# Kernel optimization log

Measured on AMD Instinct MI355X. Metric: run time of the kernel, lower is better.

Reference implementation:

```python
import jax, jax.numpy as jnp
import numpy as np

N_NODES = 50000
N_EDGES = 800000
D_IN = 128
D_OUT = 128


def setup_inputs() -> dict:
    key = jax.random.key(0)
    k_x, k_r, k_c, k_v, k_w = jax.random.split(key, 5)
    x = jax.random.normal(k_x, (N_NODES, D_IN), dtype=jnp.float32)
    edge_row = jax.random.randint(k_r, (N_EDGES,), 0, N_NODES)  # destination nodes
    edge_col = jax.random.randint(k_c, (N_EDGES,), 0, N_NODES)  # source nodes
    edge_val = jax.random.uniform(k_v, (N_EDGES,), dtype=jnp.float32)
    W = jax.random.normal(k_w, (D_OUT, D_IN), dtype=jnp.float32) * (1.0 / np.sqrt(D_IN))
    bias = jnp.zeros((D_OUT,), dtype=jnp.float32)
    return {"x": x, "edge_row": edge_row, "edge_col": edge_col,
            "edge_val": edge_val, "W": W, "bias": bias}


def reference(x, edge_row, edge_col, edge_val, W, bias):
    # support = linear(x)   (nn.Linear with bias=False: x @ W.T)
    support = jnp.einsum('ni,oi->no', x, W)  # [N, D_OUT]
    # out = sparse.mm(adj, support): gather source rows, scale by edge value,
    # scatter-add into destination rows.
    msgs = edge_val[:, None] * support[edge_col]  # [E, D_OUT]
    out = jax.ops.segment_sum(msgs, edge_row, num_segments=N_NODES)
    return out + bias
```

## Files before the change

kernel.cpp:

```cpp
#include <hip/hip_runtime.h>
#include <hip/hip_bf16.h>


constexpr int D     = 128;
constexpr int NPB   = 64;
constexpr int CAP   = 2048;
constexpr int C1    = 2048;
constexpr int BT    = 1024;
constexpr int NBMAX = 1024;

__device__ inline unsigned int bf1(float f) {
    unsigned int u = __float_as_uint(f);
    return (u + 0x7fffu + ((u >> 16) & 1u)) >> 16;
}
__device__ inline unsigned int cvt2(float a, float b) {
    __hip_bfloat162 h = __float22bfloat162_rn(float2{a, b});
    return *reinterpret_cast<unsigned int*>(&h);
}
__device__ inline float bflo(unsigned int u) { return __uint_as_float(u << 16); }
__device__ inline float bfhi(unsigned int u) { return __uint_as_float(u & 0xffff0000u); }

__global__ __launch_bounds__(256) void fused_gemm_bin_kernel(
        const float* __restrict__ x, const float* __restrict__ W,
        const int* __restrict__ erow, const int* __restrict__ ecol,
        const float* __restrict__ eval,
        int* __restrict__ gcursor, int2* __restrict__ coarse,
        unsigned short* __restrict__ supb,
        int n_edges, int nb, int n_nodes, int bin_blocks) {
    if ((int)blockIdx.x < bin_blocks) {
        __shared__ int bkcnt[NBMAX];
        __shared__ int bkoff[NBMAX];
        __shared__ int wsum[4];
        __shared__ int gbase[NBMAX];
        __shared__ unsigned short slotbk[C1];
        __shared__ int2 stage[C1];
        const int t = threadIdx.x;
        const int base = blockIdx.x * C1;
        const int m = min(C1, n_edges - base);

        for (int i = t; i < NBMAX; i += 256) bkcnt[i] = 0;
        __syncthreads();

        constexpr int EPT = C1 / 256;
        int  bk[EPT], rank[EPT];
        int2 pk[EPT];
#pragma unroll
        for (int j = 0; j < EPT; ++j) {
            int i = t + j * 256;
            bk[j] = -1;
            if (i < m) {
                int e = base + i;
                int dst = erow[e];
                int b = dst / NPB;
                bk[j] = b;
                rank[j] = atomicAdd(&bkcnt[b], 1);
                pk[j] = make_int2(ecol[e] | ((dst & (NPB - 1)) << 20),
                                  __float_as_int(eval[e]));
            }
        }
        __syncthreads();

        {
            const int w = t >> 6, l = t & 63;
            const int b0 = 4 * t;
            int c0 = bkcnt[b0], c1 = bkcnt[b0 + 1];
            int c2 = bkcnt[b0 + 2], c3 = bkcnt[b0 + 3];
            int s = c0 + c1 + c2 + c3;
            int inc = s;
#pragma unroll
            for (int o = 1; o < 64; o <<= 1) {
                int u = __shfl_up(inc, o, 64);
                if (l >= o) inc += u;
            }
            if (l == 63) wsum[w] = inc;
            __syncthreads();
            if (t < 4) {
                int v = wsum[t];
                int winc = v;
#pragma unroll
                for (int o = 1; o < 4; o <<= 1) {
                    int u = __shfl_up(winc, o, 4);
                    if (t >= o) winc += u;
                }
                wsum[t] = winc - v;
            }
            __syncthreads();
            int p = inc - s + wsum[w];
            bkoff[b0]     = p;
            bkoff[b0 + 1] = p + c0;
            bkoff[b0 + 2] = p + c0 + c1;
            bkoff[b0 + 3] = p + c0 + c1 + c2;
        }
        __syncthreads();

#pragma unroll
        for (int j = 0; j < EPT; ++j) {
            if (bk[j] >= 0) {
                int s2 = bkoff[bk[j]] + rank[j];
                stage[s2] = pk[j];
                slotbk[s2] = (unsigned short)bk[j];
            }
        }
        for (int i = t; i < nb; i += 256) {
            int c = bkcnt[i];
            gbase[i] = (c > 0) ? (i * CAP + atomicAdd(&gcursor[i], c)) : 0;
        }
        __syncthreads();

        for (int i = t; i < m; i += 256) {
            int b = slotbk[i];
            int p = gbase[b] + (i - bkoff[b]);
            if (p < (b + 1) * CAP) coarse[p] = stage[i];
        }
    } else {
        using frag  = __attribute__((ext_vector_type(8))) short;
        using f32x4 = __attribute__((ext_vector_type(4))) float;
        union FU { uint4 u; frag f; };
        const int wv = threadIdx.x >> 6;
        const int lane = threadIdx.x & 63;
        const int mm = lane & 15, quad = lane >> 4;
        const int row0 = (blockIdx.x - bin_blocks) * 128 + wv * 32;
        const int r0 = min(row0 + mm, n_nodes - 1);
        const int r1 = min(row0 + 16 + mm, n_nodes - 1);

        frag a0[4], a1[4];
#pragma unroll
        for (int kf = 0; kf < 4; ++kf) {
            const float4* xp0 = (const float4*)(x + (size_t)r0 * D + kf * 32 + quad * 8);
            float4 p = xp0[0], q = xp0[1];
            FU t;
            t.u.x = cvt2(p.x, p.y); t.u.y = cvt2(p.z, p.w);
            t.u.z = cvt2(q.x, q.y); t.u.w = cvt2(q.z, q.w);
            a0[kf] = t.f;
            const float4* xp1 = (const float4*)(x + (size_t)r1 * D + kf * 32 + quad * 8);
            p = xp1[0]; q = xp1[1];
            t.u.x = cvt2(p.x, p.y); t.u.y = cvt2(p.z, p.w);
            t.u.z = cvt2(q.x, q.y); t.u.w = cvt2(q.z, q.w);
            a1[kf] = t.f;
        }

        f32x4 acc0[8], acc1[8];
#pragma unroll
        for (int ct = 0; ct < 8; ++ct) {
            acc0[ct] = (f32x4){0.f, 0.f, 0.f, 0.f};
            acc1[ct] = (f32x4){0.f, 0.f, 0.f, 0.f};
        }

#pragma unroll
        for (int ct = 0; ct < 8; ++ct) {
            const float* wrow = W + (size_t)(ct * 16 + mm) * D;
#pragma unroll
            for (int kf = 0; kf < 4; ++kf) {
                const float4* wp = (const float4*)(wrow + kf * 32 + quad * 8);
                float4 p = wp[0], q = wp[1];
                FU tb;
                tb.u.x = cvt2(p.x, p.y); tb.u.y = cvt2(p.z, p.w);
                tb.u.z = cvt2(q.x, q.y); tb.u.w = cvt2(q.z, q.w);
                frag b = tb.f;
                acc0[ct] = __builtin_amdgcn_mfma_f32_16x16x32_bf16(a0[kf], b, acc0[ct], 0, 0, 0);
                acc1[ct] = __builtin_amdgcn_mfma_f32_16x16x32_bf16(a1[kf], b, acc1[ct], 0, 0, 0);
            }
        }

#pragma unroll
        for (int ct = 0; ct < 8; ++ct) {
#pragma unroll
            for (int r = 0; r < 4; ++r) {
                int rr0 = row0 + quad * 4 + r;
                if (rr0 < n_nodes)
                    supb[(size_t)rr0 * D + ct * 16 + mm] = (unsigned short)bf1(acc0[ct][r]);
                int rr1 = row0 + 16 + quad * 4 + r;
                if (rr1 < n_nodes)
                    supb[(size_t)rr1 * D + ct * 16 + mm] = (unsigned short)bf1(acc1[ct][r]);
            }
        }
    }
}

__global__ __launch_bounds__(BT) void sortgather_kernel(const int* __restrict__ gcursor,
                                                        const int2* __restrict__ coarse,
                                                        const unsigned short* __restrict__ supb,
                                                        const float* __restrict__ bias,
                                                        float* __restrict__ out,
                                                        int n_nodes) {
    __shared__ int ncnt[NPB];
    __shared__ int noff[NPB];
    __shared__ int ncur[NPB];
    __shared__ int2 sorted[CAP];
    const int t = threadIdx.x;
    const int b = blockIdx.x;
    const int node0 = b * NPB;
    const int m = min(gcursor[b], CAP);
    const int2* src = coarse + (size_t)b * CAP;

    if (t < NPB) ncnt[t] = 0;
    __syncthreads();

    for (int i = t; i < m; i += BT)
        atomicAdd(&ncnt[(src[i].x >> 20) & (NPB - 1)], 1);
    __syncthreads();

    if (t < NPB) {
        int v = ncnt[t];
        int inc = v;
        for (int o = 1; o < NPB; o <<= 1) {
            int u = __shfl_up(inc, o, 64);
            if (t >= o) inc += u;
        }
        noff[t] = inc - v;
        ncur[t] = inc - v;
    }
    __syncthreads();

    for (int i = t; i < m; i += BT) {
        int2 e = src[i];
        int dl = (e.x >> 20) & (NPB - 1);
        int p = atomicAdd(&ncur[dl], 1);
        sorted[p] = make_int2(e.x & 0xFFFFF, e.y);
    }
    __syncthreads();

    const int qw = t >> 4;
    const int l16 = t & 15;
    const int node = node0 + qw;
    if (node >= n_nodes) return;
    const int beg = noff[qw];
    const int end = beg + ncnt[qw];

    const float4* b4 = (const float4*)(bias + l16 * 8);
    float4 acc0 = b4[0], acc1 = b4[1];

    int e = beg;
    for (; e + 1 < end; e += 2) {
        int2 d0 = sorted[e], d1 = sorted[e + 1];
        uint4 u0 = *(const uint4*)(supb + (size_t)d0.x * D + l16 * 8);
        uint4 u1 = *(const uint4*)(supb + (size_t)d1.x * D + l16 * 8);
        float v0 = __int_as_float(d0.y), v1 = __int_as_float(d1.y);
        acc0.x += v0 * bflo(u0.x) + v1 * bflo(u1.x);
        acc0.y += v0 * bfhi(u0.x) + v1 * bfhi(u1.x);
        acc0.z += v0 * bflo(u0.y) + v1 * bflo(u1.y);
        acc0.w += v0 * bfhi(u0.y) + v1 * bfhi(u1.y);
        acc1.x += v0 * bflo(u0.z) + v1 * bflo(u1.z);
        acc1.y += v0 * bfhi(u0.z) + v1 * bfhi(u1.z);
        acc1.z += v0 * bflo(u0.w) + v1 * bflo(u1.w);
        acc1.w += v0 * bfhi(u0.w) + v1 * bfhi(u1.w);
    }
    if (e < end) {
        int2 d0 = sorted[e];
        uint4 u0 = *(const uint4*)(supb + (size_t)d0.x * D + l16 * 8);
        float v0 = __int_as_float(d0.y);
        acc0.x += v0 * bflo(u0.x); acc0.y += v0 * bfhi(u0.x);
        acc0.z += v0 * bflo(u0.y); acc0.w += v0 * bfhi(u0.y);
        acc1.x += v0 * bflo(u0.z); acc1.y += v0 * bfhi(u0.z);
        acc1.z += v0 * bflo(u0.w); acc1.w += v0 * bfhi(u0.w);
    }
    float4* o4 = (float4*)(out + (size_t)node * D + l16 * 8);
    o4[0] = acc0;
    o4[1] = acc1;
}

__global__ __launch_bounds__(256) void init_out_kernel(float4* __restrict__ out4,
                                                       const float4* __restrict__ bias4,
                                                       int total4) {
    int i = blockIdx.x * 256 + threadIdx.x;
    if (i < total4) out4[i] = bias4[i & 31];
}

__global__ __launch_bounds__(256) void scatter_fb_kernel(const int* __restrict__ erow,
                                                         const int* __restrict__ ecol,
                                                         const float* __restrict__ eval,
                                                         const unsigned short* __restrict__ supb,
                                                         float* __restrict__ out,
                                                         int n_edges) {
    int e = blockIdx.x * 8 + (threadIdx.x >> 5);
    if (e >= n_edges) return;
    int lane = threadIdx.x & 31;
    int src = ecol[e], dst = erow[e];
    float v = eval[e];
    const unsigned short* sp = supb + (size_t)src * D + lane * 4;
    float* op = out + (size_t)dst * D + lane * 4;
#pragma unroll
    for (int j = 0; j < 4; ++j)
        atomicAdd(op + j, v * __uint_as_float(((unsigned)sp[j]) << 16));
}

static inline size_t align_up(size_t v, size_t a) { return (v + a - 1) & ~(a - 1); }

extern "C" void kernel_launch(void* const* d_in, const int* in_sizes, int n_in,
                              void* d_out, int out_size, void* d_ws, size_t ws_size,
                              hipStream_t stream) {
    const float* x    = (const float*)d_in[0];
    const int*   erow = (const int*)d_in[1];
    const int*   ecol = (const int*)d_in[2];
    const float* eval = (const float*)d_in[3];
    const float* W    = (const float*)d_in[4];
    const float* bias = (const float*)d_in[5];
    float* out = (float*)d_out;

    const int n_nodes = in_sizes[0] / D;
    const int n_edges = in_sizes[1];
    const int nb = (n_nodes + NPB - 1) / NPB;

    char* base = (char*)d_ws;
    size_t off = 0;
    unsigned short* supb = (unsigned short*)(base + off); off = align_up(off + (size_t)n_nodes * D * 2, 256);
    int*  gcursor = (int*)(base + off);  off = align_up(off + (size_t)nb * 4, 256);
    int2* coarse  = (int2*)(base + off); off = align_up(off + (size_t)nb * CAP * 8, 256);

    const bool fast = (n_nodes < (1 << 20)) && (nb <= NBMAX) && (off <= ws_size);
    const int gemm_blocks = (n_nodes + 127) / 128;
    const int bin_blocks = fast ? (n_edges + C1 - 1) / C1 : 0;

    if (fast)
        hipMemsetAsync(gcursor, 0, (size_t)nb * 4, stream);

    fused_gemm_bin_kernel<<<bin_blocks + gemm_blocks, 256, 0, stream>>>(
        x, W, erow, ecol, eval, gcursor, coarse, supb,
        n_edges, nb, n_nodes, bin_blocks);

    if (fast) {
        sortgather_kernel<<<nb, BT, 0, stream>>>(
            gcursor, coarse, supb, bias, out, n_nodes);
    } else {
        int total4 = n_nodes * (D / 4);
        init_out_kernel<<<(total4 + 255) / 256, 256, 0, stream>>>(
            (float4*)out, (const float4*)bias, total4);
        scatter_fb_kernel<<<(n_edges + 7) / 8, 256, 0, stream>>>(
            erow, ecol, eval, supb, out, n_edges);
    }
}
```

Before: 144.8 us.

## Replace per-node sort-and-gather with fixed-point LDS atomic accumulation

The second-stage kernel no longer counting-sorts each bin's edges by destination node. Instead every wave streams edges and accumulates scaled bf16 products into a 64x128 integer accumulator in LDS using fixed-point integer atomics, then converts to float and adds bias. This removes the histogram, scan and scatter passes and the per-node load imbalance. In exchange it adds two LDS atomics per element, uses 4-byte gathers instead of 16-byte gathers, and introduces fixed-point quantization and possible overflow for large sums.

```diff
diff --git a/kernel.cpp b/kernel.cpp
--- a/kernel.cpp
+++ b/kernel.cpp
@@ -19,6 +19,9 @@
 }
 __device__ inline float bflo(unsigned int u) { return __uint_as_float(u << 16); }
 __device__ inline float bfhi(unsigned int u) { return __uint_as_float(u & 0xffff0000u); }
+
+constexpr float FXS  = 2097152.0f;
+constexpr float FXSI = 1.0f / 2097152.0f;
 
 __global__ __launch_bounds__(256) void fused_gemm_bin_kernel(
         const float* __restrict__ x, const float* __restrict__ W,
@@ -177,86 +180,70 @@
     }
 }
 
-__global__ __launch_bounds__(BT) void sortgather_kernel(const int* __restrict__ gcursor,
-                                                        const int2* __restrict__ coarse,
-                                                        const unsigned short* __restrict__ supb,
-                                                        const float* __restrict__ bias,
-                                                        float* __restrict__ out,
-                                                        int n_nodes) {
-    __shared__ int ncnt[NPB];
-    __shared__ int noff[NPB];
-    __shared__ int ncur[NPB];
-    __shared__ int2 sorted[CAP];
+__global__ __launch_bounds__(BT) void accgather_kernel(const int* __restrict__ gcursor,
+                                                       const int2* __restrict__ coarse,
+                                                       const unsigned short* __restrict__ supb,
+                                                       const float* __restrict__ bias,
+                                                       float* __restrict__ out,
+                                                       int n_nodes) {
+    __shared__ int  acc[NPB * D];
+    __shared__ int2 elist[CAP];
     const int t = threadIdx.x;
     const int b = blockIdx.x;
     const int node0 = b * NPB;
     const int m = min(gcursor[b], CAP);
     const int2* src = coarse + (size_t)b * CAP;
 
-    if (t < NPB) ncnt[t] = 0;
+    for (int i = t; i < NPB * D / 4; i += BT)
+        ((int4*)acc)[i] = int4{0, 0, 0, 0};
+    for (int i = t; i < m; i += BT) elist[i] = src[i];
     __syncthreads();
 
-    for (int i = t; i < m; i += BT)
-        atomicAdd(&ncnt[(src[i].x >> 20) & (NPB - 1)], 1);
+    const int wv = t >> 6;
+    const int c  = t & 63;
+
+    int e = wv;
+    for (; e + 48 < m; e += 64) {
+        int2 d0 = elist[e], d1 = elist[e + 16], d2 = elist[e + 32], d3 = elist[e + 48];
+        unsigned int u0 = ((const unsigned int*)(supb + ((size_t)(d0.x & 0xFFFFF) << 7)))[c];
+        unsigned int u1 = ((const unsigned int*)(supb + ((size_t)(d1.x & 0xFFFFF) << 7)))[c];
+        unsigned int u2 = ((const unsigned int*)(supb + ((size_t)(d2.x & 0xFFFFF) << 7)))[c];
+        unsigned int u3 = ((const unsigned int*)(supb + ((size_t)(d3.x & 0xFFFFF) << 7)))[c];
+        float v0 = __int_as_float(d0.y) * FXS, v1 = __int_as_float(d1.y) * FXS;
+        float v2 = __int_as_float(d2.y) * FXS, v3 = __int_as_float(d3.y) * FXS;
+        int* a0 = acc + ((d0.x >> 20) & 63) * D + 2 * c;
+        int* a1 = acc + ((d1.x >> 20) & 63) * D + 2 * c;
+        int* a2 = acc + ((d2.x >> 20) & 63) * D + 2 * c;
+        int* a3 = acc + ((d3.x >> 20) & 63) * D + 2 * c;
+        atomicAdd(a0,     __float2int_rn(bflo(u0) * v0));
+        atomicAdd(a0 + 1, __float2int_rn(bfhi(u0) * v0));
+        atomicAdd(a1,     __float2int_rn(bflo(u1) * v1));
+        atomicAdd(a1 + 1, __float2int_rn(bfhi(u1) * v1));
+        atomicAdd(a2,     __float2int_rn(bflo(u2) * v2));
+        atomicAdd(a2 + 1, __float2int_rn(bfhi(u2) * v2));
+        atomicAdd(a3,     __float2int_rn(bflo(u3) * v3));
+        atomicAdd(a3 + 1, __float2int_rn(bfhi(u3) * v3));
+    }
+    for (; e < m; e += 16) {
+        int2 d0 = elist[e];
+        unsigned int u0 = ((const unsigned int*)(supb + ((size_t)(d0.x & 0xFFFFF) << 7)))[c];
+        float v0 = __int_as_float(d0.y) * FXS;
+        int* a0 = acc + ((d0.x >> 20) & 63) * D + 2 * c;
+        atomicAdd(a0,     __float2int_rn(bflo(u0) * v0));
+        atomicAdd(a0 + 1, __float2int_rn(bfhi(u0) * v0));
+    }
     __syncthreads();
 
-    if (t < NPB) {
-        int v = ncnt[t];
-        int inc = v;
-        for (int o = 1; o < NPB; o <<= 1) {
-            int u = __shfl_up(inc, o, 64);
-            if (t >= o) inc += u;
-        }
-        noff[t] = inc - v;
-        ncur[t] = inc - v;
-    }
-    __syncthreads();
-
-    for (int i = t; i < m; i += BT) {
-        int2 e = src[i];
-        int dl = (e.x >> 20) & (NPB - 1);
-        int p = atomicAdd(&ncur[dl], 1);
-        sorted[p] = make_int2(e.x & 0xFFFFF, e.y);
-    }
-    __syncthreads();
-
-    const int qw = t >> 4;
-    const int l16 = t & 15;
-    const int node = node0 + qw;
-    if (node >= n_nodes) return;
-    const int beg = noff[qw];
-    const int end = beg + ncnt[qw];
-
-    const float4* b4 = (const float4*)(bias + l16 * 8);
-    float4 acc0 = b4[0], acc1 = b4[1];
-
-    int e = beg;
-    for (; e + 1 < end; e += 2) {
-        int2 d0 = sorted[e], d1 = sorted[e + 1];
-        uint4 u0 = *(const uint4*)(supb + (size_t)d0.x * D + l16 * 8);
-        uint4 u1 = *(const uint4*)(supb + (size_t)d1.x * D + l16 * 8);
-        float v0 = __int_as_float(d0.y), v1 = __int_as_float(d1.y);
-        acc0.x += v0 * bflo(u0.x) + v1 * bflo(u1.x);
-        acc0.y += v0 * bfhi(u0.x) + v1 * bfhi(u1.x);
-        acc0.z += v0 * bflo(u0.y) + v1 * bflo(u1.y);
-        acc0.w += v0 * bfhi(u0.y) + v1 * bfhi(u1.y);
-        acc1.x += v0 * bflo(u0.z) + v1 * bflo(u1.z);
-        acc1.y += v0 * bfhi(u0.z) + v1 * bfhi(u1.z);
-        acc1.z += v0 * bflo(u0.w) + v1 * bflo(u1.w);
-        acc1.w += v0 * bfhi(u0.w) + v1 * bfhi(u1.w);
-    }
-    if (e < end) {
-        int2 d0 = sorted[e];
-        uint4 u0 = *(const uint4*)(supb + (size_t)d0.x * D + l16 * 8);
-        float v0 = __int_as_float(d0.y);
-        acc0.x += v0 * bflo(u0.x); acc0.y += v0 * bfhi(u0.x);
-        acc0.z += v0 * bflo(u0.y); acc0.w += v0 * bfhi(u0.y);
-        acc1.x += v0 * bflo(u0.z); acc1.y += v0 * bfhi(u0.z);
-        acc1.z += v0 * bflo(u0.w); acc1.w += v0 * bfhi(u0.w);
-    }
-    float4* o4 = (float4*)(out + (size_t)node * D + l16 * 8);
-    o4[0] = acc0;
-    o4[1] = acc1;
+    const int nvalid = min(NPB, n_nodes - node0);
+    for (int i = t; i < nvalid * (D / 4); i += BT) {
+        int node = i >> 5;
+        int q = i & 31;
+        int4 a = ((const int4*)acc)[node * 32 + q];
+        float4 bb = ((const float4*)bias)[q];
+        float4 r{(float)a.x * FXSI + bb.x, (float)a.y * FXSI + bb.y,
+                 (float)a.z * FXSI + bb.z, (float)a.w * FXSI + bb.w};
+        ((float4*)(out + (size_t)(node0 + node) * D))[q] = r;
+    }
 }
 
 __global__ __launch_bounds__(256) void init_out_kernel(float4* __restrict__ out4,
@@ -319,7 +306,7 @@
         n_edges, nb, n_nodes, bin_blocks);
 
     if (fast) {
-        sortgather_kernel<<<nb, BT, 0, stream>>>(
+        accgather_kernel<<<nb, BT, 0, stream>>>(
             gcursor, coarse, supb, bias, out, n_nodes);
     } else {
         int total4 = n_nodes * (D / 4);
```

Measured after the change: 151.1 us. 1.04x slower.

## Stage bf16 W in swizzled LDS per GEMM block and halve rows per block

Applied to the files above, without the earlier changes.

Each GEMM block now converts the full W matrix to bf16 once into shared memory, stored with an XOR swizzle, and every wave reads its B fragments from LDS. Before, every wave reloaded and reconverted W from global memory for each tile. Rows per block drop from 128 to 64 (16 per wave instead of 32), which doubles the GEMM block count and lowers per-thread register use. The bin and GEMM shared-memory layouts are merged into a union so the fused kernel's LDS footprint stays bounded. The cost is an extra barrier and more blocks, each of which converts W again.

```diff
diff --git a/kernel.cpp b/kernel.cpp
--- a/kernel.cpp
+++ b/kernel.cpp
@@ -19,6 +19,19 @@
 }
 __device__ inline float bflo(unsigned int u) { return __uint_as_float(u << 16); }
 __device__ inline float bfhi(unsigned int u) { return __uint_as_float(u & 0xffff0000u); }
+
+struct BinSmem {
+    int bkcnt[NBMAX];
+    int bkoff[NBMAX];
+    int wsum[4];
+    int gbase[NBMAX];
+    unsigned short slotbk[C1];
+    int2 stage[C1];
+};
+struct GemmSmem {
+    uint4 wb[2048];
+};
+union SmemU { BinSmem b; GemmSmem g; };
 
 __global__ __launch_bounds__(256) void fused_gemm_bin_kernel(
         const float* __restrict__ x, const float* __restrict__ W,
@@ -27,18 +40,13 @@
         int* __restrict__ gcursor, int2* __restrict__ coarse,
         unsigned short* __restrict__ supb,
         int n_edges, int nb, int n_nodes, int bin_blocks) {
+    __shared__ SmemU sm;
+    const int t = threadIdx.x;
     if ((int)blockIdx.x < bin_blocks) {
-        __shared__ int bkcnt[NBMAX];
-        __shared__ int bkoff[NBMAX];
-        __shared__ int wsum[4];
-        __shared__ int gbase[NBMAX];
-        __shared__ unsigned short slotbk[C1];
-        __shared__ int2 stage[C1];
-        const int t = threadIdx.x;
         const int base = blockIdx.x * C1;
         const int m = min(C1, n_edges - base);
 
-        for (int i = t; i < NBMAX; i += 256) bkcnt[i] = 0;
+        for (int i = t; i < NBMAX; i += 256) sm.b.bkcnt[i] = 0;
         __syncthreads();
 
         constexpr int EPT = C1 / 256;
@@ -53,7 +61,7 @@
                 int dst = erow[e];
                 int b = dst / NPB;
                 bk[j] = b;
-                rank[j] = atomicAdd(&bkcnt[b], 1);
+                rank[j] = atomicAdd(&sm.b.bkcnt[b], 1);
                 pk[j] = make_int2(ecol[e] | ((dst & (NPB - 1)) << 20),
                                   __float_as_int(eval[e]));
             }
@@ -63,8 +71,8 @@
         {
             const int w = t >> 6, l = t & 63;
             const int b0 = 4 * t;
-            int c0 = bkcnt[b0], c1 = bkcnt[b0 + 1];
-            int c2 = bkcnt[b0 + 2], c3 = bkcnt[b0 + 3];
+            int c0 = sm.b.bkcnt[b0], c1 = sm.b.bkcnt[b0 + 1];
+            int c2 = sm.b.bkcnt[b0 + 2], c3 = sm.b.bkcnt[b0 + 3];
             int s = c0 + c1 + c2 + c3;
             int inc = s;
 #pragma unroll
@@ -72,106 +80,103 @@
                 int u = __shfl_up(inc, o, 64);
                 if (l >= o) inc += u;
             }
-            if (l == 63) wsum[w] = inc;
+            if (l == 63) sm.b.wsum[w] = inc;
             __syncthreads();
             if (t < 4) {
-                int v = wsum[t];
+                int v = sm.b.wsum[t];
                 int winc = v;
 #pragma unroll
                 for (int o = 1; o < 4; o <<= 1) {
                     int u = __shfl_up(winc, o, 4);
                     if (t >= o) winc += u;
                 }
-                wsum[t] = winc - v;
+                sm.b.wsum[t] = winc - v;
             }
             __syncthreads();
-            int p = inc - s + wsum[w];
-            bkoff[b0]     = p;
-            bkoff[b0 + 1] = p + c0;
-            bkoff[b0 + 2] = p + c0 + c1;
-            bkoff[b0 + 3] = p + c0 + c1 + c2;
+            int p = inc - s + sm.b.wsum[w];
+            sm.b.bkoff[b0]     = p;
+            sm.b.bkoff[b0 + 1] = p + c0;
+            sm.b.bkoff[b0 + 2] = p + c0 + c1;
+            sm.b.bkoff[b0 + 3] = p + c0 + c1 + c2;
         }
         __syncthreads();
 
 #pragma unroll
         for (int j = 0; j < EPT; ++j) {
             if (bk[j] >= 0) {
-                int s2 = bkoff[bk[j]] + rank[j];
-                stage[s2] = pk[j];
-                slotbk[s2] = (unsigned short)bk[j];
+                int s2 = sm.b.bkoff[bk[j]] + rank[j];
+                sm.b.stage[s2] = pk[j];
+                sm.b.slotbk[s2] = (unsigned short)bk[j];
             }
         }
         for (int i = t; i < nb; i += 256) {
-            int c = bkcnt[i];
-            gbase[i] = (c > 0) ? (i * CAP + atomicAdd(&gcursor[i], c)) : 0;
+            int c = sm.b.bkcnt[i];
+            sm.b.gbase[i] = (c > 0) ? (i * CAP + atomicAdd(&gcursor[i], c)) : 0;
         }
         __syncthreads();
 
         for (int i = t; i < m; i += 256) {
-            int b = slotbk[i];
-            int p = gbase[b] + (i - bkoff[b]);
-            if (p < (b + 1) * CAP) coarse[p] = stage[i];
+            int b = sm.b.slotbk[i];
+            int p = sm.b.gbase[b] + (i - sm.b.bkoff[b]);
+            if (p < (b + 1) * CAP) coarse[p] = sm.b.stage[i];
         }
     } else {
         using frag  = __attribute__((ext_vector_type(8))) short;
         using f32x4 = __attribute__((ext_vector_type(4))) float;
         union FU { uint4 u; frag f; };
-        const int wv = threadIdx.x >> 6;
-        const int lane = threadIdx.x & 63;
+        const int gb = blockIdx.x - bin_blocks;
+        const int wv = t >> 6;
+        const int lane = t & 63;
         const int mm = lane & 15, quad = lane >> 4;
-        const int row0 = (blockIdx.x - bin_blocks) * 128 + wv * 32;
+        const int row0 = gb * 64 + wv * 16;
         const int r0 = min(row0 + mm, n_nodes - 1);
-        const int r1 = min(row0 + 16 + mm, n_nodes - 1);
-
-        frag a0[4], a1[4];
+
+        frag a[4];
 #pragma unroll
         for (int kf = 0; kf < 4; ++kf) {
-            const float4* xp0 = (const float4*)(x + (size_t)r0 * D + kf * 32 + quad * 8);
-            float4 p = xp0[0], q = xp0[1];
-            FU t;
-            t.u.x = cvt2(p.x, p.y); t.u.y = cvt2(p.z, p.w);
-            t.u.z = cvt2(q.x, q.y); t.u.w = cvt2(q.z, q.w);
-            a0[kf] = t.f;
-            const float4* xp1 = (const float4*)(x + (size_t)r1 * D + kf * 32 + quad * 8);
-            p = xp1[0]; q = xp1[1];
-            t.u.x = cvt2(p.x, p.y); t.u.y = cvt2(p.z, p.w);
-            t.u.z = cvt2(q.x, q.y); t.u.w = cvt2(q.z, q.w);
-            a1[kf] = t.f;
-        }
-
-        f32x4 acc0[8], acc1[8];
+            const float4* xp = (const float4*)(x + (size_t)r0 * D + kf * 32 + quad * 8);
+            float4 p = xp[0], q = xp[1];
+            FU tu;
+            tu.u.x = cvt2(p.x, p.y); tu.u.y = cvt2(p.z, p.w);
+            tu.u.z = cvt2(q.x, q.y); tu.u.w = cvt2(q.z, q.w);
+            a[kf] = tu.f;
+        }
+
+#pragma unroll
+        for (int j = 0; j < 8; ++j) {
+            int c = t + j * 256;
+            int o = c >> 4, k16 = c & 15;
+            const float4* wp = (const float4*)(W + (size_t)o * D + k16 * 8);
+            float4 p = wp[0], q = wp[1];
+            uint4 r;
+            r.x = cvt2(p.x, p.y); r.y = cvt2(p.z, p.w);
+            r.z = cvt2(q.x, q.y); r.w = cvt2(q.z, q.w);
+            sm.g.wb[(o << 4) + (k16 ^ (o & 7))] = r;
+        }
+        __syncthreads();
+
+        f32x4 acc[8];
+#pragma unroll
+        for (int ct = 0; ct < 8; ++ct) acc[ct] = (f32x4){0.f, 0.f, 0.f, 0.f};
+
 #pragma unroll
         for (int ct = 0; ct < 8; ++ct) {
-            acc0[ct] = (f32x4){0.f, 0.f, 0.f, 0.f};
-            acc1[ct] = (f32x4){0.f, 0.f, 0.f, 0.f};
+            const int o = ct * 16 + mm;
+#pragma unroll
+            for (int kf = 0; kf < 4; ++kf) {
+                FU bu;
+                bu.u = sm.g.wb[(o << 4) + ((kf * 4 + quad) ^ (mm & 7))];
+                acc[ct] = __builtin_amdgcn_mfma_f32_16x16x32_bf16(a[kf], bu.f, acc[ct], 0, 0, 0);
+            }
         }
 
 #pragma unroll
         for (int ct = 0; ct < 8; ++ct) {
-            const float* wrow = W + (size_t)(ct * 16 + mm) * D;
-#pragma unroll
-            for (int kf = 0; kf < 4; ++kf) {
-                const float4* wp = (const float4*)(wrow + kf * 32 + quad * 8);
-                float4 p = wp[0], q = wp[1];
-                FU tb;
-                tb.u.x = cvt2(p.x, p.y); tb.u.y = cvt2(p.z, p.w);
-                tb.u.z = cvt2(q.x, q.y); tb.u.w = cvt2(q.z, q.w);
-                frag b = tb.f;
-                acc0[ct] = __builtin_amdgcn_mfma_f32_16x16x32_bf16(a0[kf], b, acc0[ct], 0, 0, 0);
-                acc1[ct] = __builtin_amdgcn_mfma_f32_16x16x32_bf16(a1[kf], b, acc1[ct], 0, 0, 0);
-            }
-        }
-
-#pragma unroll
-        for (int ct = 0; ct < 8; ++ct) {
 #pragma unroll
             for (int r = 0; r < 4; ++r) {
-                int rr0 = row0 + quad * 4 + r;
-                if (rr0 < n_nodes)
-                    supb[(size_t)rr0 * D + ct * 16 + mm] = (unsigned short)bf1(acc0[ct][r]);
-                int rr1 = row0 + 16 + quad * 4 + r;
-                if (rr1 < n_nodes)
-                    supb[(size_t)rr1 * D + ct * 16 + mm] = (unsigned short)bf1(acc1[ct][r]);
+                int rr = row0 + quad * 4 + r;
+                if (rr < n_nodes)
+                    supb[(size_t)rr * D + ct * 16 + mm] = (unsigned short)bf1(acc[ct][r]);
             }
         }
     }
@@ -308,7 +313,7 @@
     int2* coarse  = (int2*)(base + off); off = align_up(off + (size_t)nb * CAP * 8, 256);
 
     const bool fast = (n_nodes < (1 << 20)) && (nb <= NBMAX) && (off <= ws_size);
-    const int gemm_blocks = (n_nodes + 127) / 128;
+    const int gemm_blocks = (n_nodes + 63) / 64;
     const int bin_blocks = fast ? (n_edges + C1 - 1) / C1 : 0;
 
     if (fast)
```

Measured after the change: 137.6 us, median of 2. 1.05x faster.
